# Kernel tuning notes

Measured on AMD Instinct MI355X. Metric: run time of the kernel, lower is better.

## Reference

```python
import jax, jax.numpy as jnp
import numpy as np

B, N, D = 1, 2048, 1024
L, H, DH = 4, 16, 64
INNER = H * DH            # 1024, == D
FF = int(D * 4.0)         # 4096 (GEGLU inner)
SCALE = DH ** -0.5
LN_EPS = 1e-5


def setup_inputs() -> dict:
    key = jax.random.key(0)
    ks = jax.random.split(key, 8)
    w = 0.02
    inp = {
        'x': jax.random.normal(ks[0], (B, N, D), jnp.float32),
        'mask': jnp.ones((B, N), dtype=bool),
        # stacked per-layer params (leading dim L)
        'Wqkv': jax.random.normal(ks[1], (L, D, 3 * INNER), jnp.float32) * w,
        'Wo': jax.random.normal(ks[2], (L, INNER, D), jnp.float32) * w,
        'bo': jnp.zeros((L, D), jnp.float32),
        'ln1_g': jnp.ones((L, D), jnp.float32),
        'ln1_b': jnp.zeros((L, D), jnp.float32),
        'ln2_g': jnp.ones((L, D), jnp.float32),
        'ln2_b': jnp.zeros((L, D), jnp.float32),
        'ls1': jnp.full((L, D), 0.1, jnp.float32),  # LayerScale init_eps=0.1 (depth<=18)
        'ls2': jnp.full((L, D), 0.1, jnp.float32),
        'W1': jax.random.normal(ks[3], (L, D, 2 * FF), jnp.float32) * w,
        'b1': jnp.zeros((L, 2 * FF), jnp.float32),
        'W2': jax.random.normal(ks[4], (L, FF, D), jnp.float32) * w,
        'b2': jnp.zeros((L, D), jnp.float32),
    }
    return inp


def _layernorm(x, g, b):
    mu = jnp.mean(x, axis=-1, keepdims=True)
    var = jnp.mean(jnp.square(x - mu), axis=-1, keepdims=True)
    return (x - mu) * jax.lax.rsqrt(var + LN_EPS) * g + b


def _forward(x, mask, Wqkv, Wo, bo, ln1_g, ln1_b, ln2_g, ln2_b, ls1, ls2, W1, b1, W2, b2):
    n = x.shape[1]
    causal = jnp.arange(n)[None, :] > jnp.arange(n)[:, None]  # True = masked
    valid = mask[:, None, None, :] & ~causal[None, None]       # (B,1,N,N) True = keep
    for l in range(L):
        # --- attention sublayer: x + LayerScale(PreNorm(Attn))(x) ---
        h = _layernorm(x, ln1_g[l], ln1_b[l])
        qkv = h @ Wqkv[l]                                      # (B,N,3*INNER)
        q, k, v = jnp.split(qkv, 3, axis=-1)
        q = q.reshape(B, n, H, DH).transpose(0, 2, 1, 3) * SCALE
        k = k.reshape(B, n, H, DH).transpose(0, 2, 1, 3)
        v = v.reshape(B, n, H, DH).transpose(0, 2, 1, 3)
        dots = jnp.einsum('bhid,bhjd->bhij', q, k)             # (B,H,N,N)
        neg = -jnp.finfo(dots.dtype).max
        dots = jnp.where(valid, dots, neg)
        attn = jax.nn.softmax(dots, axis=-1)                   # stable_softmax, temp=1
        o = jnp.einsum('bhij,bhjd->bhid', attn, v)
        o = o.transpose(0, 2, 1, 3).reshape(B, n, INNER)
        o = o @ Wo[l] + bo[l]
        x = x + o * ls1[l]
        # --- feedforward sublayer: x + LayerScale(PreNorm(GEGLU-FFN))(x) ---
        h = _layernorm(x, ln2_g[l], ln2_b[l])
        u = h @ W1[l] + b1[l]                                  # (B,N,2*FF)
        a, g = jnp.split(u, 2, axis=-1)
        f = (a * jax.nn.gelu(g, approximate=False)) @ W2[l] + b2[l]
        x = x + f * ls2[l]
    return x


def reference(x, mask, Wqkv, Wo, bo, ln1_g, ln1_b, ln2_g, ln2_b, ls1, ls2, W1, b1, W2, b2):
    return _forward(x, mask, Wqkv, Wo, bo, ln1_g, ln1_b, ln2_g, ln2_b, ls1, ls2, W1, b1, W2, b2)
```

## Files before the change

kernel.cpp:

```cpp
#include <hip/hip_runtime.h>
#include <hip/hip_bf16.h>
#include <math.h>

#define LN_EPS 1e-5f
#define ATT_SCALE 0.125f

typedef __bf16 bf16x8 __attribute__((ext_vector_type(8)));
typedef float f32x4 __attribute__((ext_vector_type(4)));

__device__ __forceinline__ unsigned short f2bf(float f){
  unsigned int u = __builtin_bit_cast(unsigned int, f);
  u += 0x7fffu + ((u >> 16) & 1u);
  return (unsigned short)(u >> 16);
}
__device__ __forceinline__ float bfbits2f(unsigned int lo16){
  return __builtin_bit_cast(float, lo16 << 16);
}

__global__ __launch_bounds__(256) void ln_kernel(
    const float* __restrict__ X, const float* __restrict__ g,
    const float* __restrict__ b, unsigned short* __restrict__ H)
{
  __shared__ float red[4];
  int row = blockIdx.x, t = threadIdx.x;
  const float4 xv = ((const float4*)(X + (size_t)row*1024))[t];
  float s = xv.x + xv.y + xv.z + xv.w;
  #pragma unroll
  for (int o=32;o;o>>=1) s += __shfl_down(s,o);
  if ((t&63)==0) red[t>>6] = s;
  __syncthreads();
  float mu = (red[0]+red[1]+red[2]+red[3]) * (1.f/1024.f);
  __syncthreads();
  float dx = xv.x-mu, dy = xv.y-mu, dz = xv.z-mu, dw = xv.w-mu;
  float s2 = dx*dx+dy*dy+dz*dz+dw*dw;
  #pragma unroll
  for (int o=32;o;o>>=1) s2 += __shfl_down(s2,o);
  if ((t&63)==0) red[t>>6] = s2;
  __syncthreads();
  float var = (red[0]+red[1]+red[2]+red[3]) * (1.f/1024.f);
  float rs = rsqrtf(var + LN_EPS);
  const float4 gv = ((const float4*)g)[t];
  const float4 bv = ((const float4*)b)[t];
  ushort4 o4;
  o4.x = f2bf(dx*rs*gv.x + bv.x);
  o4.y = f2bf(dy*rs*gv.y + bv.y);
  o4.z = f2bf(dz*rs*gv.z + bv.z);
  o4.w = f2bf(dw*rs*gv.w + bv.w);
  ((ushort4*)(H + (size_t)row*1024))[t] = o4;
}

template<int SK, int DO_LN>
__global__ __launch_bounds__(256) void redln_kernel(
    const float* __restrict__ P, float* __restrict__ X,
    const float* __restrict__ bias, const float* __restrict__ scale,
    const float* __restrict__ g, const float* __restrict__ b,
    unsigned short* __restrict__ H)
{
  __shared__ float red[4];
  int row = blockIdx.x, t = threadIdx.x;
  size_t off = (size_t)row*1024 + t*4;
  float4 xv = *(const float4*)(X + off);
  float4 pv = *(const float4*)(P + off);
  #pragma unroll
  for (int c=1;c<SK;c++){
    float4 q = *(const float4*)(P + (size_t)c*2048*1024 + off);
    pv.x+=q.x; pv.y+=q.y; pv.z+=q.z; pv.w+=q.w;
  }
  const float4 bv = ((const float4*)bias)[t];
  const float4 sv = ((const float4*)scale)[t];
  xv.x += (pv.x+bv.x)*sv.x;
  xv.y += (pv.y+bv.y)*sv.y;
  xv.z += (pv.z+bv.z)*sv.z;
  xv.w += (pv.w+bv.w)*sv.w;
  *(float4*)(X + off) = xv;
  if (DO_LN){
    float s = xv.x + xv.y + xv.z + xv.w;
    #pragma unroll
    for (int o=32;o;o>>=1) s += __shfl_down(s,o);
    if ((t&63)==0) red[t>>6] = s;
    __syncthreads();
    float mu = (red[0]+red[1]+red[2]+red[3]) * (1.f/1024.f);
    __syncthreads();
    float dx = xv.x-mu, dy = xv.y-mu, dz = xv.z-mu, dw = xv.w-mu;
    float s2 = dx*dx+dy*dy+dz*dz+dw*dw;
    #pragma unroll
    for (int o=32;o;o>>=1) s2 += __shfl_down(s2,o);
    if ((t&63)==0) red[t>>6] = s2;
    __syncthreads();
    float var = (red[0]+red[1]+red[2]+red[3]) * (1.f/1024.f);
    float rs = rsqrtf(var + LN_EPS);
    const float4 gv = ((const float4*)g)[t];
    const float4 lbv = ((const float4*)b)[t];
    ushort4 o4;
    o4.x = f2bf(dx*rs*gv.x + lbv.x);
    o4.y = f2bf(dy*rs*gv.y + lbv.y);
    o4.z = f2bf(dz*rs*gv.z + lbv.z);
    o4.w = f2bf(dw*rs*gv.w + lbv.w);
    ((ushort4*)(H + (size_t)row*1024))[t] = o4;
  }
}

__global__ __launch_bounds__(256) void trc_kernel(
    const float* __restrict__ W, unsigned short* __restrict__ WT, int K, int N)
{
  __shared__ float tile[64][65];
  int n0 = blockIdx.x*64, k0 = blockIdx.y*64;
  int t = threadIdx.x;
  int tx = t & 63, ty = t >> 6;
  #pragma unroll
  for (int p=0;p<16;p++){
    int r = ty*16+p;
    tile[r][tx] = W[(size_t)(k0+r)*N + n0 + tx];
  }
  __syncthreads();
  int kc = t & 31, tb = t >> 5;
  #pragma unroll
  for (int p=0;p<8;p++){
    int nr = tb + p*8;
    unsigned int lo = f2bf(tile[2*kc][nr]);
    unsigned int hi = f2bf(tile[2*kc+1][nr]);
    ((unsigned int*)(WT + (size_t)(n0+nr)*K + k0))[kc] = lo | (hi<<16);
  }
}

__global__ __launch_bounds__(256) void trc_w1_kernel(
    const float* __restrict__ W, unsigned short* __restrict__ WT)
{
  __shared__ float tile[64][65];
  int n0 = blockIdx.x*64, k0 = blockIdx.y*64;
  int ca = (n0>>5)*16;
  int t = threadIdx.x;
  int tx = t & 63, ty = t >> 6;
  #pragma unroll
  for (int p=0;p<16;p++){
    int r = ty*16+p;
    int col = (tx < 32) ? (ca + tx) : (ca + 4064 + tx);
    tile[r][tx] = W[(size_t)(k0+r)*8192 + col];
  }
  __syncthreads();
  int kc = t & 31, tb = t >> 5;
  #pragma unroll
  for (int p=0;p<8;p++){
    int nr = tb + p*8;
    int rr = nr & 31;
    int vcol = (nr>>5)*16 + (rr&15) + ((rr>>4)<<5);
    unsigned int lo = f2bf(tile[2*kc][vcol]);
    unsigned int hi = f2bf(tile[2*kc+1][vcol]);
    ((unsigned int*)(WT + (size_t)(n0+nr)*1024 + k0))[kc] = lo | (hi<<16);
  }
}

template<int MODE>
__global__ __launch_bounds__(256) void gemm_bt(
    const unsigned short* __restrict__ A, const unsigned short* __restrict__ BT,
    int M, int N, int K,
    float* __restrict__ Xres, unsigned short* __restrict__ Obf,
    const float* __restrict__ bias, const float* __restrict__ scale)
{
  __shared__ unsigned short Asm[2][128*64];
  __shared__ unsigned short Bsm[2][128*64];
  int t = threadIdx.x;
  int lane = t & 63;
  int w = t >> 6, wm = w >> 1, wn = w & 1;

  int nwg = gridDim.x * gridDim.y;
  int wg = blockIdx.y * gridDim.x + blockIdx.x;
  int cpx = nwg >> 3;
  int swz = (wg & 7) * cpx + (wg >> 3);
  int bn = swz % gridDim.x, bm = swz / gridDim.x;

  f32x4 acc[4][4] = {};
  int ktBeg = 0, ktEnd = K >> 6;
  if (MODE == 3){
    int per = (K >> 6) / gridDim.z;
    ktBeg = blockIdx.z * per;
    ktEnd = ktBeg + per;
  }

  int srow = t >> 3, ssc = t & 7;
  auto STAGE = [&](int kt, int buf){
    #pragma unroll
    for (int c=0;c<4;c++){
      int row = c*32 + srow;
      int gc = ssc ^ (row & 7);
      const unsigned short* sa = A  + (size_t)(bm*128 + row)*K + kt*64 + gc*8;
      const unsigned short* sb = BT + (size_t)(bn*128 + row)*K + kt*64 + gc*8;
      __builtin_amdgcn_global_load_lds(
        (const __attribute__((address_space(1))) unsigned int*)sa,
        (__attribute__((address_space(3))) unsigned int*)(&Asm[buf][(c*256 + (t & ~63))*8]),
        16, 0, 0);
      __builtin_amdgcn_global_load_lds(
        (const __attribute__((address_space(1))) unsigned int*)sb,
        (__attribute__((address_space(3))) unsigned int*)(&Bsm[buf][(c*256 + (t & ~63))*8]),
        16, 0, 0);
    }
  };

  STAGE(ktBeg, 0);
  __syncthreads();
  int cur = 0;
  for (int kt = ktBeg; kt < ktEnd; ++kt){
    if (kt + 1 < ktEnd) STAGE(kt + 1, cur ^ 1);
    #pragma unroll
    for (int kk=0;kk<2;kk++){
      bf16x8 aF[4], bF[4];
      #pragma unroll
      for (int m=0;m<4;m++){
        int row = wm*64 + m*16 + (lane&15);
        int ch = kk*4 + (lane>>4);
        aF[m] = *(const bf16x8*)&Asm[cur][row*64 + (ch ^ (row&7))*8];
      }
      #pragma unroll
      for (int n=0;n<4;n++){
        int row = wn*64 + n*16 + (lane&15);
        int ch = kk*4 + (lane>>4);
        bF[n] = *(const bf16x8*)&Bsm[cur][row*64 + (ch ^ (row&7))*8];
      }
      __builtin_amdgcn_s_setprio(1);
      #pragma unroll
      for (int m=0;m<4;m++)
        #pragma unroll
        for (int n=0;n<4;n++)
          acc[m][n] = __builtin_amdgcn_mfma_f32_16x16x32_bf16(aF[m], bF[n], acc[m][n], 0,0,0);
      __builtin_amdgcn_s_setprio(0);
    }
    __syncthreads();
    cur ^= 1;
  }

  int colg = lane & 15;
  if (MODE==4){
    float b1a[2], b1g[2];
    #pragma unroll
    for (int p=0;p<2;p++){
      int oc = (bn*4 + wn*2 + p)*16 + colg;
      b1a[p] = bias[oc];
      b1g[p] = bias[oc + 4096];
    }
    #pragma unroll
    for (int m=0;m<4;m++){
      int gr0 = bm*128 + wm*64 + m*16 + (lane>>4)*4;
      #pragma unroll
      for (int p=0;p<2;p++){
        int ocol = (bn*4 + wn*2 + p)*16 + colg;
        #pragma unroll
        for (int j=0;j<4;j++){
          float va = acc[m][2*p][j]   + b1a[p];
          float vg = acc[m][2*p+1][j] + b1g[p];
          float f = va * (0.5f * vg * (1.f + erff(vg * 0.70710678118f)));
          Obf[(size_t)(gr0+j)*4096 + ocol] = f2bf(f);
        }
      }
    }
    return;
  }
  #pragma unroll
  for (int m=0;m<4;m++){
    int gr0 = bm*128 + wm*64 + m*16 + (lane>>4)*4;
    #pragma unroll
    for (int n=0;n<4;n++){
      int gc = bn*128 + wn*64 + n*16 + colg;
      #pragma unroll
      for (int j=0;j<4;j++){
        int gr = gr0 + j;
        float v = acc[m][n][j];
        if (MODE==0){
          Obf[(size_t)gr*N + gc] = f2bf(v);
        } else {
          Xres[(size_t)blockIdx.z*((size_t)M*N) + (size_t)gr*N + gc] = v;
        }
      }
    }
  }
}

__global__ __launch_bounds__(256) void vtr_kernel(
    const unsigned short* __restrict__ qkv, unsigned short* __restrict__ VT)
{
  __shared__ unsigned int tile[64][33];
  int h = blockIdx.y;
  int n0 = blockIdx.x * 64;
  int t = threadIdx.x;
  #pragma unroll
  for (int p=0;p<8;p++){
    int idx = p*256 + t;
    int r = idx >> 5, c = idx & 31;
    tile[r][c] = *(const unsigned int*)(qkv + (size_t)(n0+r)*3072 + 2048 + h*64 + c*2);
  }
  __syncthreads();
  #pragma unroll
  for (int p=0;p<8;p++){
    int idx = p*256 + t;
    int d = idx >> 5, c = idx & 31;
    unsigned int a = tile[2*c][d>>1];
    unsigned int b = tile[2*c+1][d>>1];
    unsigned int lo = (d&1) ? (a>>16) : (a & 0xffffu);
    unsigned int hi = (d&1) ? (b>>16) : (b & 0xffffu);
    *(unsigned int*)(VT + (size_t)h*131072 + (size_t)d*2048 + n0 + c*2) = lo | (hi<<16);
  }
}

__global__ __launch_bounds__(256) void flash_attn(
    const unsigned short* __restrict__ qkv,
    const unsigned short* __restrict__ VT,
    unsigned short* __restrict__ O)
{
  __shared__ unsigned short Klds[2][64*64];
  __shared__ unsigned short Vlds[2][64*64];
  __shared__ unsigned short Plds[4][16*72];
  __shared__ float fbuf[4][16];
  __shared__ float lbuf[4][16];

  int t = threadIdx.x;
  int lane = t & 63;
  int w = t >> 6;
  int q15 = lane & 15, l16 = lane >> 4;

  int bid = blockIdx.x;
  int half = bid >> 8, idx = bid & 255;
  int h = (idx >> 5) + half*8;
  int qt = half ? (31 - (idx & 31)) : (idx & 31);
  int q0 = qt * 64;

  bf16x8 qF[2];
  int qrow = q0 + w*16 + q15;
  #pragma unroll
  for (int db=0; db<2; db++)
    qF[db] = *(const bf16x8*)(qkv + (size_t)qrow*3072 + h*64 + db*32 + l16*8);

  int srow = t >> 3, ssc = t & 7;
  auto STAGE = [&](int kt, int buf){
    int k0 = kt*64;
    #pragma unroll
    for (int c=0;c<2;c++){
      int row = c*32 + srow;
      int gc = ssc ^ (row & 7);
      const unsigned short* sk = qkv + (size_t)(k0+row)*3072 + 1024 + h*64 + gc*8;
      const unsigned short* sv = VT + (size_t)h*131072 + (size_t)row*2048 + k0 + gc*8;
      __builtin_amdgcn_global_load_lds(
        (const __attribute__((address_space(1))) unsigned int*)sk,
        (__attribute__((address_space(3))) unsigned int*)(&Klds[buf][(c*256 + (t & ~63))*8]),
        16, 0, 0);
      __builtin_amdgcn_global_load_lds(
        (const __attribute__((address_space(1))) unsigned int*)sv,
        (__attribute__((address_space(3))) unsigned int*)(&Vlds[buf][(c*256 + (t & ~63))*8]),
        16, 0, 0);
    }
  };

  f32x4 o[4] = {};
  float m_run = -1e30f, l_run = 0.f;

  STAGE(0, 0);
  __syncthreads();
  int cur = 0;
  for (int kt = 0; kt <= qt; ++kt){
    if (kt < qt) STAGE(kt + 1, cur ^ 1);

    f32x4 s[4] = {};
    #pragma unroll
    for (int km=0;km<4;km++){
      #pragma unroll
      for (int db=0;db<2;db++){
        int row = km*16 + q15;
        int ch = db*4 + l16;
        bf16x8 kF = *(const bf16x8*)&Klds[cur][row*64 + (ch ^ (row&7))*8];
        s[km] = __builtin_amdgcn_mfma_f32_16x16x32_bf16(kF, qF[db], s[km], 0,0,0);
      }
    }

    bool diag = (kt == qt);
    float pmax = -1e30f;
    #pragma unroll
    for (int km=0;km<4;km++){
      #pragma unroll
      for (int j=0;j<4;j++){
        float sv = s[km][j] * ATT_SCALE;
        if (diag){
          int kg = km*16 + l16*4 + j;
          int qg = w*16 + q15;
          if (kg > qg) sv = -1e30f;
        }
        s[km][j] = sv;
        pmax = fmaxf(pmax, sv);
      }
    }
    pmax = fmaxf(pmax, __shfl_xor(pmax, 16));
    pmax = fmaxf(pmax, __shfl_xor(pmax, 32));

    float m_new = fmaxf(m_run, pmax);
    float f = __expf(m_run - m_new);

    float lsum = 0.f;
    #pragma unroll
    for (int km=0;km<4;km++){
      float p0 = __expf(s[km][0]-m_new);
      float p1 = __expf(s[km][1]-m_new);
      float p2 = __expf(s[km][2]-m_new);
      float p3 = __expf(s[km][3]-m_new);
      lsum += (p0+p1)+(p2+p3);
      unsigned int u0 = (unsigned int)f2bf(p0) | ((unsigned int)f2bf(p1)<<16);
      unsigned int u1 = (unsigned int)f2bf(p2) | ((unsigned int)f2bf(p3)<<16);
      *(uint2*)&Plds[w][q15*72 + km*16 + l16*4] = make_uint2(u0,u1);
    }
    lsum += __shfl_xor(lsum,16);
    lsum += __shfl_xor(lsum,32);
    l_run = l_run * f + lsum;
    m_run = m_new;

    if (l16 == 0) fbuf[w][q15] = f;
    f32x4 fv = *(f32x4*)&fbuf[w][l16*4];
    #pragma unroll
    for (int n=0;n<4;n++) o[n] *= fv;

    #pragma unroll
    for (int kb=0;kb<2;kb++){
      bf16x8 aP = *(const bf16x8*)&Plds[w][q15*72 + kb*32 + l16*8];
      #pragma unroll
      for (int n=0;n<4;n++){
        int row = n*16 + q15;
        int ch = kb*4 + l16;
        bf16x8 vF = *(const bf16x8*)&Vlds[cur][row*64 + (ch ^ (row&7))*8];
        o[n] = __builtin_amdgcn_mfma_f32_16x16x32_bf16(aP, vF, o[n], 0,0,0);
      }
    }
    __syncthreads();
    cur ^= 1;
  }

  if (l16 == 0) lbuf[w][q15] = 1.f / l_run;
  f32x4 lv = *(f32x4*)&lbuf[w][l16*4];

  #pragma unroll
  for (int n=0;n<4;n++){
    #pragma unroll
    for (int j=0;j<4;j++){
      int row = q0 + w*16 + l16*4 + j;
      int col = h*64 + n*16 + q15;
      O[(size_t)row*1024 + col] = f2bf(o[n][j]*lv[j]);
    }
  }
}

extern "C" void kernel_launch(void* const* d_in, const int* in_sizes, int n_in,
                              void* d_out, int out_size, void* d_ws, size_t ws_size,
                              hipStream_t stream)
{
  (void)in_sizes; (void)n_in; (void)out_size; (void)ws_size;
  const float* x_in = (const float*)d_in[0];
  const float* Wqkv = (const float*)d_in[2];
  const float* Wo   = (const float*)d_in[3];
  const float* bo   = (const float*)d_in[4];
  const float* ln1g = (const float*)d_in[5];
  const float* ln1b = (const float*)d_in[6];
  const float* ln2g = (const float*)d_in[7];
  const float* ln2b = (const float*)d_in[8];
  const float* ls1  = (const float*)d_in[9];
  const float* ls2  = (const float*)d_in[10];
  const float* W1   = (const float*)d_in[11];
  const float* b1   = (const float*)d_in[12];
  const float* W2   = (const float*)d_in[13];
  const float* b2   = (const float*)d_in[14];
  float* X = (float*)d_out;

  char* ws = (char*)d_ws;
  unsigned short* WT  = (unsigned short*)(ws);
  unsigned short* hb  = (unsigned short*)(ws + (16u<<20));
  unsigned short* qu  = (unsigned short*)(ws + (20u<<20));
  unsigned short* VTg = (unsigned short*)(ws + (36u<<20));
  unsigned short* of  = (unsigned short*)(ws + (52u<<20));
  float* PT  = (float*)(ws + (20u<<20));

  hipMemcpyAsync(d_out, (const void*)x_in, (size_t)2048*1024*4,
                 hipMemcpyDeviceToDevice, stream);

  for (int l = 0; l < 4; ++l){
    if (l == 0)
      ln_kernel<<<2048,256,0,stream>>>(X, ln1g, ln1b, hb);
    trc_kernel<<<dim3(3072/64,1024/64),256,0,stream>>>(Wqkv + (size_t)l*1024*3072, WT, 1024, 3072);
    gemm_bt<0><<<dim3(3072/128,2048/128),256,0,stream>>>(hb, WT, 2048,3072,1024,
        nullptr, qu, nullptr, nullptr);
    vtr_kernel<<<dim3(32,16),256,0,stream>>>(qu, VTg);
    flash_attn<<<512,256,0,stream>>>(qu, VTg, of);
    trc_kernel<<<dim3(1024/64,1024/64),256,0,stream>>>(Wo + (size_t)l*1024*1024, WT, 1024, 1024);
    gemm_bt<3><<<dim3(1024/128,2048/128,2),256,0,stream>>>(of, WT, 2048,1024,1024,
        PT, nullptr, nullptr, nullptr);
    redln_kernel<2,1><<<2048,256,0,stream>>>(PT, X, bo + l*1024, ls1 + l*1024,
        ln2g + l*1024, ln2b + l*1024, hb);
    trc_w1_kernel<<<dim3(8192/64,1024/64),256,0,stream>>>(W1 + (size_t)l*1024*8192, WT);
    gemm_bt<4><<<dim3(8192/128,2048/128),256,0,stream>>>(hb, WT, 2048,8192,1024,
        nullptr, of, b1 + (size_t)l*8192, nullptr);
    trc_kernel<<<dim3(1024/64,4096/64),256,0,stream>>>(W2 + (size_t)l*4096*1024, WT, 4096, 1024);
    gemm_bt<3><<<dim3(1024/128,2048/128,4),256,0,stream>>>(of, WT, 2048,1024,4096,
        PT, nullptr, nullptr, nullptr);
    if (l < 3)
      redln_kernel<4,1><<<2048,256,0,stream>>>(PT, X, b2 + l*1024, ls2 + l*1024,
          ln1g + (l+1)*1024, ln1b + (l+1)*1024, hb);
    else
      redln_kernel<4,0><<<2048,256,0,stream>>>(PT, X, b2 + l*1024, ls2 + l*1024,
          nullptr, nullptr, nullptr);
  }
}
```

Baseline: 830.0 us.

## Store split-K partials in bf16, disable swizzle for some GEMMs, remap attention blocks

Split-K GEMM partial sums are now written as bf16 rather than fp32, and the reduction kernel reads bf16. This halves the partial-sum traffic in both the GEMM epilogue and the reduce step. Workgroup swizzling becomes a template switch and is turned off for the QKV and W1 GEMMs. The flash attention block-to-(head, query tile) mapping is also changed to interleave heads and pair causal tiles differently. Rounding the partials to bf16 before summing loses some accuracy.

```diff
diff --git a/kernel.cpp b/kernel.cpp
--- a/kernel.cpp
+++ b/kernel.cpp
@@ -51,7 +51,7 @@
 
 template<int SK, int DO_LN>
 __global__ __launch_bounds__(256) void redln_kernel(
-    const float* __restrict__ P, float* __restrict__ X,
+    const unsigned short* __restrict__ P, float* __restrict__ X,
     const float* __restrict__ bias, const float* __restrict__ scale,
     const float* __restrict__ g, const float* __restrict__ b,
     unsigned short* __restrict__ H)
@@ -60,11 +60,17 @@
   int row = blockIdx.x, t = threadIdx.x;
   size_t off = (size_t)row*1024 + t*4;
   float4 xv = *(const float4*)(X + off);
-  float4 pv = *(const float4*)(P + off);
+  float4 pv;
+  {
+    uint2 u = *(const uint2*)(P + off);
+    pv.x = bfbits2f(u.x & 0xffffu); pv.y = bfbits2f(u.x >> 16);
+    pv.z = bfbits2f(u.y & 0xffffu); pv.w = bfbits2f(u.y >> 16);
+  }
   #pragma unroll
   for (int c=1;c<SK;c++){
-    float4 q = *(const float4*)(P + (size_t)c*2048*1024 + off);
-    pv.x+=q.x; pv.y+=q.y; pv.z+=q.z; pv.w+=q.w;
+    uint2 u = *(const uint2*)(P + (size_t)c*2048*1024 + off);
+    pv.x += bfbits2f(u.x & 0xffffu); pv.y += bfbits2f(u.x >> 16);
+    pv.z += bfbits2f(u.y & 0xffffu); pv.w += bfbits2f(u.y >> 16);
   }
   const float4 bv = ((const float4*)bias)[t];
   const float4 sv = ((const float4*)scale)[t];
@@ -150,12 +156,12 @@
   }
 }
 
-template<int MODE>
+template<int MODE, int SWZ>
 __global__ __launch_bounds__(256) void gemm_bt(
     const unsigned short* __restrict__ A, const unsigned short* __restrict__ BT,
     int M, int N, int K,
-    float* __restrict__ Xres, unsigned short* __restrict__ Obf,
-    const float* __restrict__ bias, const float* __restrict__ scale)
+    unsigned short* __restrict__ Obf,
+    const float* __restrict__ bias)
 {
   __shared__ unsigned short Asm[2][128*64];
   __shared__ unsigned short Bsm[2][128*64];
@@ -163,11 +169,16 @@
   int lane = t & 63;
   int w = t >> 6, wm = w >> 1, wn = w & 1;
 
-  int nwg = gridDim.x * gridDim.y;
-  int wg = blockIdx.y * gridDim.x + blockIdx.x;
-  int cpx = nwg >> 3;
-  int swz = (wg & 7) * cpx + (wg >> 3);
-  int bn = swz % gridDim.x, bm = swz / gridDim.x;
+  int bn, bm;
+  if (SWZ){
+    int nwg = gridDim.x * gridDim.y;
+    int wg = blockIdx.y * gridDim.x + blockIdx.x;
+    int cpx = nwg >> 3;
+    int swz = (wg & 7) * cpx + (wg >> 3);
+    bn = swz % gridDim.x; bm = swz / gridDim.x;
+  } else {
+    bn = blockIdx.x; bm = blockIdx.y;
+  }
 
   f32x4 acc[4][4] = {};
   int ktBeg = 0, ktEnd = K >> 6;
@@ -267,7 +278,7 @@
         if (MODE==0){
           Obf[(size_t)gr*N + gc] = f2bf(v);
         } else {
-          Xres[(size_t)blockIdx.z*((size_t)M*N) + (size_t)gr*N + gc] = v;
+          Obf[(size_t)blockIdx.z*((size_t)M*N) + (size_t)gr*N + gc] = f2bf(v);
         }
       }
     }
@@ -317,9 +328,10 @@
   int q15 = lane & 15, l16 = lane >> 4;
 
   int bid = blockIdx.x;
-  int half = bid >> 8, idx = bid & 255;
-  int h = (idx >> 5) + half*8;
-  int qt = half ? (31 - (idx & 31)) : (idx & 31);
+  int x = bid & 7, r = bid >> 3;
+  int h = 2*x + (r & 1);
+  int q = r >> 1;
+  int qt = (q < 16) ? q : 47 - q;
   int q0 = qt * 64;
 
   bf16x8 qF[2];
@@ -469,7 +481,7 @@
   unsigned short* qu  = (unsigned short*)(ws + (20u<<20));
   unsigned short* VTg = (unsigned short*)(ws + (36u<<20));
   unsigned short* of  = (unsigned short*)(ws + (52u<<20));
-  float* PT  = (float*)(ws + (20u<<20));
+  unsigned short* PTb = (unsigned short*)(ws + (20u<<20));
 
   hipMemcpyAsync(d_out, (const void*)x_in, (size_t)2048*1024*4,
                  hipMemcpyDeviceToDevice, stream);
@@ -478,26 +490,26 @@
     if (l == 0)
       ln_kernel<<<2048,256,0,stream>>>(X, ln1g, ln1b, hb);
     trc_kernel<<<dim3(3072/64,1024/64),256,0,stream>>>(Wqkv + (size_t)l*1024*3072, WT, 1024, 3072);
-    gemm_bt<0><<<dim3(3072/128,2048/128),256,0,stream>>>(hb, WT, 2048,3072,1024,
-        nullptr, qu, nullptr, nullptr);
+    gemm_bt<0,0><<<dim3(3072/128,2048/128),256,0,stream>>>(hb, WT, 2048,3072,1024,
+        qu, nullptr);
     vtr_kernel<<<dim3(32,16),256,0,stream>>>(qu, VTg);
     flash_attn<<<512,256,0,stream>>>(qu, VTg, of);
     trc_kernel<<<dim3(1024/64,1024/64),256,0,stream>>>(Wo + (size_t)l*1024*1024, WT, 1024, 1024);
-    gemm_bt<3><<<dim3(1024/128,2048/128,2),256,0,stream>>>(of, WT, 2048,1024,1024,
-        PT, nullptr, nullptr, nullptr);
-    redln_kernel<2,1><<<2048,256,0,stream>>>(PT, X, bo + l*1024, ls1 + l*1024,
+    gemm_bt<3,1><<<dim3(1024/128,2048/128,2),256,0,stream>>>(of, WT, 2048,1024,1024,
+        PTb, nullptr);
+    redln_kernel<2,1><<<2048,256,0,stream>>>(PTb, X, bo + l*1024, ls1 + l*1024,
         ln2g + l*1024, ln2b + l*1024, hb);
     trc_w1_kernel<<<dim3(8192/64,1024/64),256,0,stream>>>(W1 + (size_t)l*1024*8192, WT);
-    gemm_bt<4><<<dim3(8192/128,2048/128),256,0,stream>>>(hb, WT, 2048,8192,1024,
-        nullptr, of, b1 + (size_t)l*8192, nullptr);
+    gemm_bt<4,0><<<dim3(8192/128,2048/128),256,0,stream>>>(hb, WT, 2048,8192,1024,
+        of, b1 + (size_t)l*8192);
     trc_kernel<<<dim3(1024/64,4096/64),256,0,stream>>>(W2 + (size_t)l*4096*1024, WT, 4096, 1024);
-    gemm_bt<3><<<dim3(1024/128,2048/128,4),256,0,stream>>>(of, WT, 2048,1024,4096,
-        PT, nullptr, nullptr, nullptr);
+    gemm_bt<3,1><<<dim3(1024/128,2048/128,4),256,0,stream>>>(of, WT, 2048,1024,4096,
+        PTb, nullptr);
     if (l < 3)
-      redln_kernel<4,1><<<2048,256,0,stream>>>(PT, X, b2 + l*1024, ls2 + l*1024,
+      redln_kernel<4,1><<<2048,256,0,stream>>>(PTb, X, b2 + l*1024, ls2 + l*1024,
           ln1g + (l+1)*1024, ln1b + (l+1)*1024, hb);
     else
-      redln_kernel<4,0><<<2048,256,0,stream>>>(PT, X, b2 + l*1024, ls2 + l*1024,
+      redln_kernel<4,0><<<2048,256,0,stream>>>(PTb, X, b2 + l*1024, ls2 + l*1024,
           nullptr, nullptr, nullptr);
   }
 }
```

Measured after the change: 789.6 us. -4.9%, faster.
